# Performance work log

Measured on AMD Instinct MI355X. Metric: run time of the kernel, lower is better.

Reference implementation:

```python
import jax, jax.numpy as jnp
import numpy as np

N_NODES = 50000
N_EDGES = 800000
IN_DIM = 128
HID_DIM = 64
OUT_DIM = 64
NUM_GRAPHS = 512


def setup_inputs() -> dict:
    key = jax.random.key(0)
    ks = jax.random.split(key, 8)
    x = jax.random.normal(ks[0], (N_NODES, IN_DIM), dtype=jnp.float32)
    edge_index = jax.random.randint(ks[1], (2, N_EDGES), 0, N_NODES, dtype=jnp.int64)
    batch = jnp.sort(jax.random.randint(ks[2], (N_NODES,), 0, NUM_GRAPHS, dtype=jnp.int64))
    s1 = 1.0 / np.sqrt(IN_DIM)
    s2 = 1.0 / np.sqrt(HID_DIM)
    W1 = jax.random.uniform(ks[3], (IN_DIM, HID_DIM), jnp.float32, -s1, s1)
    b1 = jax.random.uniform(ks[4], (HID_DIM,), jnp.float32, -s1, s1)
    W2 = jax.random.uniform(ks[5], (HID_DIM, OUT_DIM), jnp.float32, -s2, s2)
    b2 = jax.random.uniform(ks[6], (OUT_DIM,), jnp.float32, -s2, s2)
    return {"x": x, "edge_index": edge_index, "batch": batch,
            "W1": W1, "b1": b1, "W2": W2, "b2": b2}


def _gcn_layer(h, W, b, src, dst, norm, n_nodes):
    # linear transform first (keeps the per-edge gather at output width)
    h = h @ W + b                      # [N, d_out]
    msg = h[src] * norm[:, None]       # [E, d_out] gathered, normalized messages
    agg = jax.ops.segment_sum(msg, dst, num_segments=n_nodes)  # scatter-add
    return jax.nn.relu(agg)


def reference(x, edge_index, batch, W1, b1, W2, b2):
    src, dst = edge_index[0], edge_index[1]
    # symmetric degree normalization: deg^{-1/2}[src] * deg^{-1/2}[dst]
    deg = jax.ops.segment_sum(jnp.ones((src.shape[0],), x.dtype), dst,
                              num_segments=N_NODES)
    dinv = jax.lax.rsqrt(jnp.maximum(deg, 1.0))
    norm = dinv[src] * dinv[dst]       # [E]

    h = _gcn_layer(x, W1, b1, src, dst, norm, N_NODES)   # dropout = identity (eval)
    h = _gcn_layer(h, W2, b2, src, dst, norm, N_NODES)

    # scatter_mean pooling over batch indices
    sums = jax.ops.segment_sum(h, batch, num_segments=NUM_GRAPHS)
    cnts = jax.ops.segment_sum(jnp.ones((N_NODES,), h.dtype), batch,
                               num_segments=NUM_GRAPHS)
    return sums / jnp.maximum(cnts, 1.0)[:, None]        # [NUM_GRAPHS, OUT_DIM]
```

## Files before the change

kernel.cpp:

```cpp
#include <hip/hip_runtime.h>
#include <hip/hip_fp16.h>

#define N_NODES 50000
#define N_EDGES 800000
#define IN_DIM 128
#define NUM_GRAPHS 512
#define CAP 64
#define NB 196
#define BCAP 5120
#define FILL_T 2048
#define NFILL 391
#define GEMM1_BLKS 391
#define GEMM_TILES 1563

typedef unsigned short u16;
typedef unsigned int u32;

__device__ __forceinline__ void acc_row(const uint4& v, float2& aa, float2& ab,
                                        float2& ac, float2& ad) {
    const __half2* hp = reinterpret_cast<const __half2*>(&v);
    float2 f;
    f = __half22float2(hp[0]); aa.x += f.x; aa.y += f.y;
    f = __half22float2(hp[1]); ab.x += f.x; ab.y += f.y;
    f = __half22float2(hp[2]); ac.x += f.x; ac.y += f.y;
    f = __half22float2(hp[3]); ad.x += f.x; ad.y += f.y;
}

__device__ __forceinline__ void gather_node(
    const uint4* __restrict__ H16, const u16* __restrict__ sp, int dg, int lo,
    float2& aa, float2& ab, float2& ac, float2& ad) {
    int i = 0;
    for (; i + 7 < dg; i += 8) {
        ushort4 s4a = *reinterpret_cast<const ushort4*>(sp + i);
        ushort4 s4b = *reinterpret_cast<const ushort4*>(sp + i + 4);
        uint4 v0 = H16[(size_t)s4a.x * 8 + lo];
        uint4 v1 = H16[(size_t)s4a.y * 8 + lo];
        uint4 v2 = H16[(size_t)s4a.z * 8 + lo];
        uint4 v3 = H16[(size_t)s4a.w * 8 + lo];
        uint4 v4 = H16[(size_t)s4b.x * 8 + lo];
        uint4 v5 = H16[(size_t)s4b.y * 8 + lo];
        uint4 v6 = H16[(size_t)s4b.z * 8 + lo];
        uint4 v7 = H16[(size_t)s4b.w * 8 + lo];
        acc_row(v0, aa, ab, ac, ad); acc_row(v1, aa, ab, ac, ad);
        acc_row(v2, aa, ab, ac, ad); acc_row(v3, aa, ab, ac, ad);
        acc_row(v4, aa, ab, ac, ad); acc_row(v5, aa, ab, ac, ad);
        acc_row(v6, aa, ab, ac, ad); acc_row(v7, aa, ab, ac, ad);
    }
    for (; i + 3 < dg; i += 4) {
        ushort4 s4 = *reinterpret_cast<const ushort4*>(sp + i);
        uint4 v0 = H16[(size_t)s4.x * 8 + lo];
        uint4 v1 = H16[(size_t)s4.y * 8 + lo];
        uint4 v2 = H16[(size_t)s4.z * 8 + lo];
        uint4 v3 = H16[(size_t)s4.w * 8 + lo];
        acc_row(v0, aa, ab, ac, ad); acc_row(v1, aa, ab, ac, ad);
        acc_row(v2, aa, ab, ac, ad); acc_row(v3, aa, ab, ac, ad);
    }
    for (; i < dg; ++i) {
        uint4 v = H16[(size_t)sp[i] * 8 + lo];
        acc_row(v, aa, ab, ac, ad);
    }
}

__global__ __launch_bounds__(256) void gemm1_fill_kernel(
    const float* __restrict__ X, const float* __restrict__ W,
    const float* __restrict__ bias, __half* __restrict__ Yh, int n_nodes,
    const int* __restrict__ src, const int* __restrict__ dst,
    int* __restrict__ gcursor, u32* __restrict__ packed, int n_edges) {
    __shared__ float xst[32][128];
    __shared__ float ws[32][64];
    __shared__ int hist[256], cnt2[256], goffs[256];
    const int tid = threadIdx.x;

    if (blockIdx.x & 1) {
        const int fb = blockIdx.x >> 1;
        if (fb >= NFILL) return;
        hist[tid] = 0; cnt2[tid] = 0;
        __syncthreads();
        const int base = fb * FILL_T;
        int d[8], s[8];
#pragma unroll
        for (int i = 0; i < 8; ++i) {
            int e = base + i * 256 + tid;
            if (e < n_edges) {
                d[i] = dst[e]; s[i] = src[e];
                atomicAdd(&hist[d[i] >> 8], 1);
            } else d[i] = -1;
        }
        __syncthreads();
        if (hist[tid] > 0) goffs[tid] = atomicAdd(&gcursor[tid], hist[tid]);
        __syncthreads();
#pragma unroll
        for (int i = 0; i < 8; ++i) {
            if (d[i] >= 0) {
                int b = d[i] >> 8;
                int p = goffs[b] + atomicAdd(&cnt2[b], 1);
                packed[(size_t)b * BCAP + p] = ((u32)d[i] << 16) | (u32)s[i];
            }
        }
        return;
    }

    const int idx = blockIdx.x >> 1;
    const int base = idx * 128;
    const int lane = tid & 63;
    const int w = tid >> 6;
    const int jo = lane & 7;
    const int rg = lane >> 3;
    const int rowb = w * 32 + rg * 4;

    float cc[4][8];
    {
        float4 ba = *reinterpret_cast<const float4*>(bias + jo * 8);
        float4 bb = *reinterpret_cast<const float4*>(bias + jo * 8 + 4);
#pragma unroll
        for (int r = 0; r < 4; ++r) {
            cc[r][0] = ba.x; cc[r][1] = ba.y; cc[r][2] = ba.z; cc[r][3] = ba.w;
            cc[r][4] = bb.x; cc[r][5] = bb.y; cc[r][6] = bb.z; cc[r][7] = bb.w;
        }
    }
    const float4* X4 = reinterpret_cast<const float4*>(X);
    const float4* W4 = reinterpret_cast<const float4*>(W);
    float4* ws4 = reinterpret_cast<float4*>(&ws[0][0]);

    for (int kc = 0; kc < 4; ++kc) {
        if (kc) __syncthreads();
#pragma unroll
        for (int t = 0; t < 4; ++t) {
            int i = t * 256 + tid;
            int row = i >> 3, f4 = i & 7;
            float4 v = make_float4(0.f, 0.f, 0.f, 0.f);
            if (base + row < n_nodes) v = X4[(size_t)(base + row) * 32 + kc * 8 + f4];
            int k0 = f4 * 4;
            xst[k0 + 0][row] = v.x; xst[k0 + 1][row] = v.y;
            xst[k0 + 2][row] = v.z; xst[k0 + 3][row] = v.w;
        }
#pragma unroll
        for (int t = 0; t < 2; ++t)
            ws4[t * 256 + tid] = W4[kc * 512 + t * 256 + tid];
        __syncthreads();

#pragma unroll 8
        for (int kk = 0; kk < 32; ++kk) {
            float4 xv = *reinterpret_cast<const float4*>(&xst[kk][rowb]);
            float4 wa = *reinterpret_cast<const float4*>(&ws[kk][jo * 8]);
            float4 wb = *reinterpret_cast<const float4*>(&ws[kk][jo * 8 + 4]);
            float xr[4] = {xv.x, xv.y, xv.z, xv.w};
            float wv[8] = {wa.x, wa.y, wa.z, wa.w, wb.x, wb.y, wb.z, wb.w};
#pragma unroll
            for (int r = 0; r < 4; ++r)
#pragma unroll
                for (int j = 0; j < 8; ++j) cc[r][j] += xr[r] * wv[j];
        }
    }

#pragma unroll
    for (int r = 0; r < 4; ++r) {
        int row = base + rowb + r;
        if (row < n_nodes) {
            __half2 h0 = __floats2half2_rn(cc[r][0], cc[r][1]);
            __half2 h1 = __floats2half2_rn(cc[r][2], cc[r][3]);
            __half2 h2 = __floats2half2_rn(cc[r][4], cc[r][5]);
            __half2 h3 = __floats2half2_rn(cc[r][6], cc[r][7]);
            uint4 o;
            o.x = *reinterpret_cast<u32*>(&h0); o.y = *reinterpret_cast<u32*>(&h1);
            o.z = *reinterpret_cast<u32*>(&h2); o.w = *reinterpret_cast<u32*>(&h3);
            *reinterpret_cast<uint4*>(Yh + (size_t)row * 64 + jo * 8) = o;
        }
    }
}

__global__ __launch_bounds__(256) void fine_kernel(
    const u32* __restrict__ packed, const int* __restrict__ gcursor,
    u16* __restrict__ ssorted, int* __restrict__ deg, float* __restrict__ dinv,
    __half* __restrict__ H1h,
    const int* __restrict__ batch, int* __restrict__ gstart, int n_graphs) {
    __shared__ u16 image[128 * CAP];
    __shared__ int cur[128];
    __shared__ float ds[128];
    const int tid = threadIdx.x;

    if (blockIdx.x == 2 * NB) {
        for (int g = tid; g <= n_graphs; g += 256) {
            int lo = 0, hi = N_NODES;
            while (lo < hi) {
                int mid = (lo + hi) >> 1;
                if (batch[mid] < g) lo = mid + 1; else hi = mid;
            }
            gstart[g] = lo;
        }
        return;
    }

    const int b = blockIdx.x >> 1;
    const int half = blockIdx.x & 1;
    if (tid < 128) cur[tid] = 0;
    __syncthreads();
    const int cnt = gcursor[b];
    const u32* pp = packed + (size_t)b * BCAP;
    for (int i = tid; i < cnt; i += 256) {
        u32 p = pp[i];
        int dl = (p >> 16) & 255;
        if ((dl >> 7) == half) {
            int loc = dl & 127;
            int pos = atomicAdd(&cur[loc], 1);
            if (pos < CAP) image[loc * CAP + pos] = (u16)(p & 0xffff);
        }
    }
    __syncthreads();
    const int nbase = b * 256 + half * 128;
    if (tid < 128) {
        int c = cur[tid];
        float dv = rsqrtf(fmaxf((float)c, 1.0f));
        ds[tid] = dv;
        int d = nbase + tid;
        if (d < N_NODES) { deg[d] = c; dinv[d] = dv; }
    }
    __syncthreads();
    const u32* im32 = reinterpret_cast<const u32*>(image);
    u32* out32 = reinterpret_cast<u32*>(ssorted) + (size_t)nbase * (CAP / 2);
    for (int i = tid; i < 128 * CAP / 2; i += 256) out32[i] = im32[i];
    __half2* Hp = reinterpret_cast<__half2*>(H1h) + (size_t)nbase * 32;
    const int lim = min(128, N_NODES - nbase) * 32;
    for (int i = tid; i < lim; i += 256) {
        float dv = ds[i >> 5];
        float2 f = __half22float2(Hp[i]);
        Hp[i] = __floats2half2_rn(f.x * dv, f.y * dv);
    }
}

__global__ __launch_bounds__(256) void agg_gemm_kernel(
    const __half* __restrict__ H, const u16* __restrict__ ssorted,
    const int* __restrict__ deg, const float* __restrict__ dinv,
    const float* __restrict__ W, const float* __restrict__ bias,
    __half* __restrict__ Yh, int n_nodes) {
    __shared__ float xs[32][64];
    const int tid = threadIdx.x;
    const int lane = tid & 63;
    const int w = tid >> 6;
    const int lo = lane & 7;
    const int slot = w * 8 + (lane >> 3);
    const int base = blockIdx.x * 32;
    const uint4* H16 = reinterpret_cast<const uint4*>(H);

    int node = base + slot;
    float2 aa = make_float2(0.f, 0.f), ab = make_float2(0.f, 0.f);
    float2 ac = make_float2(0.f, 0.f), ad = make_float2(0.f, 0.f);
    if (node < n_nodes) {
        int dg = min(deg[node], CAP);
        gather_node(H16, ssorted + (size_t)node * CAP, dg, lo, aa, ab, ac, ad);
        float dv = dinv[node];
        *reinterpret_cast<float4*>(&xs[slot][8 * lo]) =
            make_float4(fmaxf(aa.x * dv, 0.f), fmaxf(aa.y * dv, 0.f),
                        fmaxf(ab.x * dv, 0.f), fmaxf(ab.y * dv, 0.f));
        *reinterpret_cast<float4*>(&xs[slot][8 * lo + 4]) =
            make_float4(fmaxf(ac.x * dv, 0.f), fmaxf(ac.y * dv, 0.f),
                        fmaxf(ad.x * dv, 0.f), fmaxf(ad.y * dv, 0.f));
    } else {
        *reinterpret_cast<float4*>(&xs[slot][8 * lo]) = make_float4(0.f, 0.f, 0.f, 0.f);
        *reinterpret_cast<float4*>(&xs[slot][8 * lo + 4]) = make_float4(0.f, 0.f, 0.f, 0.f);
    }
    __syncthreads();

    float b = bias[lane];
    float c[8];
#pragma unroll
    for (int r = 0; r < 8; ++r) c[r] = b;
#pragma unroll 4
    for (int k = 0; k < 64; ++k) {
        float wv = W[k * 64 + lane];
#pragma unroll
        for (int r = 0; r < 8; ++r) c[r] += wv * xs[w * 8 + r][k];
    }
    int n0 = base + w * 8;
#pragma unroll
    for (int r = 0; r < 8; ++r)
        if (n0 + r < n_nodes)
            Yh[(size_t)(n0 + r) * 64 + lane] = __float2half(c[r] * dinv[n0 + r]);
}

__global__ __launch_bounds__(512) void agg2_pool_kernel(
    const __half* __restrict__ H, const u16* __restrict__ ssorted,
    const int* __restrict__ deg, const float* __restrict__ dinv,
    const int* __restrict__ gstart, float* __restrict__ out) {
    __shared__ float part[64][64];
    const int g = blockIdx.x;
    const int tid = threadIdx.x;
    const int lane = tid & 63;
    const int w = tid >> 6;
    const int lo = lane & 7;
    const int slot = w * 8 + (lane >> 3);
    const uint4* H16 = reinterpret_cast<const uint4*>(H);
    const int beg = gstart[g], end = gstart[g + 1];

    float2 pa = make_float2(0.f, 0.f), pb = make_float2(0.f, 0.f);
    float2 pc = make_float2(0.f, 0.f), pd = make_float2(0.f, 0.f);
    for (int node = beg + slot; node < end; node += 64) {
        int dg = min(deg[node], CAP);
        float2 aa = make_float2(0.f, 0.f), ab = make_float2(0.f, 0.f);
        float2 ac = make_float2(0.f, 0.f), ad = make_float2(0.f, 0.f);
        gather_node(H16, ssorted + (size_t)node * CAP, dg, lo, aa, ab, ac, ad);
        float dv = dinv[node];
        pa.x += fmaxf(aa.x * dv, 0.f); pa.y += fmaxf(aa.y * dv, 0.f);
        pb.x += fmaxf(ab.x * dv, 0.f); pb.y += fmaxf(ab.y * dv, 0.f);
        pc.x += fmaxf(ac.x * dv, 0.f); pc.y += fmaxf(ac.y * dv, 0.f);
        pd.x += fmaxf(ad.x * dv, 0.f); pd.y += fmaxf(ad.y * dv, 0.f);
    }
    *reinterpret_cast<float4*>(&part[slot][8 * lo]) = make_float4(pa.x, pa.y, pb.x, pb.y);
    *reinterpret_cast<float4*>(&part[slot][8 * lo + 4]) = make_float4(pc.x, pc.y, pd.x, pd.y);
    __syncthreads();
    if (tid < 64) {
        float s = 0.f;
#pragma unroll
        for (int r = 0; r < 64; ++r) s += part[r][tid];
        out[(size_t)g * 64 + tid] = s / fmaxf((float)(end - beg), 1.0f);
    }
}

extern "C" void kernel_launch(void* const* d_in, const int* in_sizes, int n_in,
                              void* d_out, int out_size, void* d_ws, size_t ws_size,
                              hipStream_t stream) {
    const float* x     = (const float*)d_in[0];
    const int*   ei    = (const int*)d_in[1];
    const int*   batch = (const int*)d_in[2];
    const float* W1    = (const float*)d_in[3];
    const float* b1    = (const float*)d_in[4];
    const float* W2    = (const float*)d_in[5];
    const float* b2    = (const float*)d_in[6];
    float* out = (float*)d_out;

    const int* srcp = ei;
    const int* dstp = ei + N_EDGES;

    __half* H1h     = (__half*)d_ws;
    __half* H2h     = H1h + (size_t)N_NODES * 64;
    float*  dinv    = (float*)(H2h + (size_t)N_NODES * 64);
    int*    deg     = (int*)(dinv + N_NODES);
    u16*    ssorted = (u16*)(deg + N_NODES);
    u32*    packed  = (u32*)(ssorted + (size_t)NB * 256 * CAP);
    int*    gcursor = (int*)(packed + (size_t)NB * BCAP);
    int*    gstart  = gcursor + 256;

    hipMemsetAsync(gcursor, 0, 256 * sizeof(int), stream);

    gemm1_fill_kernel<<<2 * NFILL, 256, 0, stream>>>(
        x, W1, b1, H1h, N_NODES, srcp, dstp, gcursor, packed, N_EDGES);

    fine_kernel<<<2 * NB + 1, 256, 0, stream>>>(
        packed, gcursor, ssorted, deg, dinv, H1h, batch, gstart, NUM_GRAPHS);

    agg_gemm_kernel<<<GEMM_TILES, 256, 0, stream>>>(
        H1h, ssorted, deg, dinv, W2, b2, H2h, N_NODES);

    agg2_pool_kernel<<<NUM_GRAPHS, 512, 0, stream>>>(
        H2h, ssorted, deg, dinv, gstart, out);
}
```

Baseline: 171.4 us.

## Replace two-pass bucketed edge sort with direct per-node atomic scatter

The two-stage build of the per-node source lists goes away: first a bucketed packed array, then a shared-memory image copied out per 256-node bucket. Each edge now does a global atomicAdd on deg[dst] and writes its source id straight into ssorted at that slot. The fine kernel becomes a light scale kernel that computes dinv and scales H1 with 16-byte vector accesses. This removes a full pass over the packed edges plus the image copy, but it adds 800k global atomics with contention and scattered 2-byte writes, and it needs a memset of the whole degree array.

```diff
diff --git a/kernel.cpp b/kernel.cpp
--- a/kernel.cpp
+++ b/kernel.cpp
@@ -6,11 +6,11 @@
 #define IN_DIM 128
 #define NUM_GRAPHS 512
 #define CAP 64
-#define NB 196
-#define BCAP 5120
-#define FILL_T 2048
-#define NFILL 391
+#define NSCAT 782
+#define SCAT_T 1024
 #define GEMM1_BLKS 391
+#define SCALE_ROWS 64
+#define SCALE_BLKS 782
 #define GEMM_TILES 1563
 
 typedef unsigned short u16;
@@ -61,46 +61,32 @@
     }
 }
 
-__global__ __launch_bounds__(256) void gemm1_fill_kernel(
+__global__ __launch_bounds__(256) void gemm1_scatter_kernel(
     const float* __restrict__ X, const float* __restrict__ W,
     const float* __restrict__ bias, __half* __restrict__ Yh, int n_nodes,
     const int* __restrict__ src, const int* __restrict__ dst,
-    int* __restrict__ gcursor, u32* __restrict__ packed, int n_edges) {
+    int* __restrict__ deg, u16* __restrict__ ssorted, int n_edges) {
     __shared__ float xst[32][128];
     __shared__ float ws[32][64];
-    __shared__ int hist[256], cnt2[256], goffs[256];
     const int tid = threadIdx.x;
 
     if (blockIdx.x & 1) {
-        const int fb = blockIdx.x >> 1;
-        if (fb >= NFILL) return;
-        hist[tid] = 0; cnt2[tid] = 0;
-        __syncthreads();
-        const int base = fb * FILL_T;
-        int d[8], s[8];
-#pragma unroll
-        for (int i = 0; i < 8; ++i) {
+        const int sb = blockIdx.x >> 1;
+        const int base = sb * SCAT_T;
+#pragma unroll
+        for (int i = 0; i < 4; ++i) {
             int e = base + i * 256 + tid;
             if (e < n_edges) {
-                d[i] = dst[e]; s[i] = src[e];
-                atomicAdd(&hist[d[i] >> 8], 1);
-            } else d[i] = -1;
-        }
-        __syncthreads();
-        if (hist[tid] > 0) goffs[tid] = atomicAdd(&gcursor[tid], hist[tid]);
-        __syncthreads();
-#pragma unroll
-        for (int i = 0; i < 8; ++i) {
-            if (d[i] >= 0) {
-                int b = d[i] >> 8;
-                int p = goffs[b] + atomicAdd(&cnt2[b], 1);
-                packed[(size_t)b * BCAP + p] = ((u32)d[i] << 16) | (u32)s[i];
+                int d = dst[e], s = src[e];
+                int pos = atomicAdd(&deg[d], 1);
+                if (pos < CAP) ssorted[(size_t)d * CAP + pos] = (u16)s;
             }
         }
         return;
     }
 
     const int idx = blockIdx.x >> 1;
+    if (idx >= GEMM1_BLKS) return;
     const int base = idx * 128;
     const int lane = tid & 63;
     const int w = tid >> 6;
@@ -169,17 +155,14 @@
     }
 }
 
-__global__ __launch_bounds__(256) void fine_kernel(
-    const u32* __restrict__ packed, const int* __restrict__ gcursor,
-    u16* __restrict__ ssorted, int* __restrict__ deg, float* __restrict__ dinv,
+__global__ __launch_bounds__(256) void scale_kernel(
+    const int* __restrict__ deg, float* __restrict__ dinv,
     __half* __restrict__ H1h,
     const int* __restrict__ batch, int* __restrict__ gstart, int n_graphs) {
-    __shared__ u16 image[128 * CAP];
-    __shared__ int cur[128];
-    __shared__ float ds[128];
+    __shared__ float ds[SCALE_ROWS];
     const int tid = threadIdx.x;
 
-    if (blockIdx.x == 2 * NB) {
+    if (blockIdx.x == SCALE_BLKS) {
         for (int g = tid; g <= n_graphs; g += 256) {
             int lo = 0, hi = N_NODES;
             while (lo < hi) {
@@ -191,40 +174,29 @@
         return;
     }
 
-    const int b = blockIdx.x >> 1;
-    const int half = blockIdx.x & 1;
-    if (tid < 128) cur[tid] = 0;
+    const int nbase = blockIdx.x * SCALE_ROWS;
+    if (tid < SCALE_ROWS) {
+        int d = nbase + tid;
+        float dv = 1.0f;
+        if (d < N_NODES) {
+            dv = rsqrtf(fmaxf((float)deg[d], 1.0f));
+            dinv[d] = dv;
+        }
+        ds[tid] = dv;
+    }
     __syncthreads();
-    const int cnt = gcursor[b];
-    const u32* pp = packed + (size_t)b * BCAP;
-    for (int i = tid; i < cnt; i += 256) {
-        u32 p = pp[i];
-        int dl = (p >> 16) & 255;
-        if ((dl >> 7) == half) {
-            int loc = dl & 127;
-            int pos = atomicAdd(&cur[loc], 1);
-            if (pos < CAP) image[loc * CAP + pos] = (u16)(p & 0xffff);
-        }
-    }
-    __syncthreads();
-    const int nbase = b * 256 + half * 128;
-    if (tid < 128) {
-        int c = cur[tid];
-        float dv = rsqrtf(fmaxf((float)c, 1.0f));
-        ds[tid] = dv;
-        int d = nbase + tid;
-        if (d < N_NODES) { deg[d] = c; dinv[d] = dv; }
-    }
-    __syncthreads();
-    const u32* im32 = reinterpret_cast<const u32*>(image);
-    u32* out32 = reinterpret_cast<u32*>(ssorted) + (size_t)nbase * (CAP / 2);
-    for (int i = tid; i < 128 * CAP / 2; i += 256) out32[i] = im32[i];
-    __half2* Hp = reinterpret_cast<__half2*>(H1h) + (size_t)nbase * 32;
-    const int lim = min(128, N_NODES - nbase) * 32;
+    uint4* Hp4 = reinterpret_cast<uint4*>(H1h) + (size_t)nbase * 8;
+    const int lim = min(SCALE_ROWS, N_NODES - nbase) * 8;
     for (int i = tid; i < lim; i += 256) {
-        float dv = ds[i >> 5];
-        float2 f = __half22float2(Hp[i]);
-        Hp[i] = __floats2half2_rn(f.x * dv, f.y * dv);
+        float dv = ds[i >> 3];
+        uint4 v = Hp4[i];
+        __half2* h = reinterpret_cast<__half2*>(&v);
+#pragma unroll
+        for (int j = 0; j < 4; ++j) {
+            float2 f = __half22float2(h[j]);
+            h[j] = __floats2half2_rn(f.x * dv, f.y * dv);
+        }
+        Hp4[i] = v;
     }
 }
 
@@ -336,17 +308,15 @@
     float*  dinv    = (float*)(H2h + (size_t)N_NODES * 64);
     int*    deg     = (int*)(dinv + N_NODES);
     u16*    ssorted = (u16*)(deg + N_NODES);
-    u32*    packed  = (u32*)(ssorted + (size_t)NB * 256 * CAP);
-    int*    gcursor = (int*)(packed + (size_t)NB * BCAP);
-    int*    gstart  = gcursor + 256;
-
-    hipMemsetAsync(gcursor, 0, 256 * sizeof(int), stream);
-
-    gemm1_fill_kernel<<<2 * NFILL, 256, 0, stream>>>(
-        x, W1, b1, H1h, N_NODES, srcp, dstp, gcursor, packed, N_EDGES);
-
-    fine_kernel<<<2 * NB + 1, 256, 0, stream>>>(
-        packed, gcursor, ssorted, deg, dinv, H1h, batch, gstart, NUM_GRAPHS);
+    int*    gstart  = (int*)(ssorted + (size_t)50176 * CAP);
+
+    hipMemsetAsync(deg, 0, N_NODES * sizeof(int), stream);
+
+    gemm1_scatter_kernel<<<2 * NSCAT, 256, 0, stream>>>(
+        x, W1, b1, H1h, N_NODES, srcp, dstp, deg, ssorted, N_EDGES);
+
+    scale_kernel<<<SCALE_BLKS + 1, 256, 0, stream>>>(
+        deg, dinv, H1h, batch, gstart, NUM_GRAPHS);
 
     agg_gemm_kernel<<<GEMM_TILES, 256, 0, stream>>>(
         H1h, ssorted, deg, dinv, W2, b2, H2h, N_NODES);
```

Measured after the change: 177.1 us. 1.03x slower.

## Use 128-node edge buckets, single-pass fill offsets, and split pooling across two blocks

Applied to the files above, without the earlier changes.

Changes edge bucketing from 256-node to 128-node buckets. Each fine block now processes exactly one bucket instead of two half-blocks both scanning the same packed list and discarding half of it. The fill phase records each edge's local slot during the histogram pass, so the second shared-memory atomic pass is gone. Pooling now uses two blocks per graph that combine through atomicAdd into a zeroed output, which raises parallelism at the cost of an extra memset and float atomics. With BCAP reduced, bucket overflow becomes a risk if edges per bucket exceed 2816.

```diff
diff --git a/kernel.cpp b/kernel.cpp
--- a/kernel.cpp
+++ b/kernel.cpp
@@ -6,8 +6,8 @@
 #define IN_DIM 128
 #define NUM_GRAPHS 512
 #define CAP 64
-#define NB 196
-#define BCAP 5120
+#define NB 392
+#define BCAP 2816
 #define FILL_T 2048
 #define NFILL 391
 #define GEMM1_BLKS 391
@@ -68,39 +68,40 @@
     int* __restrict__ gcursor, u32* __restrict__ packed, int n_edges) {
     __shared__ float xst[32][128];
     __shared__ float ws[32][64];
-    __shared__ int hist[256], cnt2[256], goffs[256];
+    __shared__ int cnt2[NB], goffs[NB];
     const int tid = threadIdx.x;
 
     if (blockIdx.x & 1) {
         const int fb = blockIdx.x >> 1;
-        if (fb >= NFILL) return;
-        hist[tid] = 0; cnt2[tid] = 0;
+        for (int i = tid; i < NB; i += 256) cnt2[i] = 0;
         __syncthreads();
         const int base = fb * FILL_T;
-        int d[8], s[8];
+        int d[8], s[8], pl[8];
 #pragma unroll
         for (int i = 0; i < 8; ++i) {
             int e = base + i * 256 + tid;
             if (e < n_edges) {
                 d[i] = dst[e]; s[i] = src[e];
-                atomicAdd(&hist[d[i] >> 8], 1);
+                pl[i] = atomicAdd(&cnt2[d[i] >> 7], 1);
             } else d[i] = -1;
         }
         __syncthreads();
-        if (hist[tid] > 0) goffs[tid] = atomicAdd(&gcursor[tid], hist[tid]);
+        for (int b = tid; b < NB; b += 256)
+            if (cnt2[b] > 0) goffs[b] = atomicAdd(&gcursor[b], cnt2[b]);
         __syncthreads();
 #pragma unroll
         for (int i = 0; i < 8; ++i) {
             if (d[i] >= 0) {
-                int b = d[i] >> 8;
-                int p = goffs[b] + atomicAdd(&cnt2[b], 1);
-                packed[(size_t)b * BCAP + p] = ((u32)d[i] << 16) | (u32)s[i];
+                int b = d[i] >> 7;
+                packed[(size_t)b * BCAP + goffs[b] + pl[i]] =
+                    ((u32)d[i] << 16) | (u32)s[i];
             }
         }
         return;
     }
 
     const int idx = blockIdx.x >> 1;
+    if (idx >= GEMM1_BLKS) return;
     const int base = idx * 128;
     const int lane = tid & 63;
     const int w = tid >> 6;
@@ -179,7 +180,7 @@
     __shared__ float ds[128];
     const int tid = threadIdx.x;
 
-    if (blockIdx.x == 2 * NB) {
+    if (blockIdx.x == NB) {
         for (int g = tid; g <= n_graphs; g += 256) {
             int lo = 0, hi = N_NODES;
             while (lo < hi) {
@@ -191,23 +192,19 @@
         return;
     }
 
-    const int b = blockIdx.x >> 1;
-    const int half = blockIdx.x & 1;
+    const int b = blockIdx.x;
     if (tid < 128) cur[tid] = 0;
     __syncthreads();
     const int cnt = gcursor[b];
     const u32* pp = packed + (size_t)b * BCAP;
     for (int i = tid; i < cnt; i += 256) {
         u32 p = pp[i];
-        int dl = (p >> 16) & 255;
-        if ((dl >> 7) == half) {
-            int loc = dl & 127;
-            int pos = atomicAdd(&cur[loc], 1);
-            if (pos < CAP) image[loc * CAP + pos] = (u16)(p & 0xffff);
-        }
-    }
-    __syncthreads();
-    const int nbase = b * 256 + half * 128;
+        int loc = (p >> 16) & 127;
+        int pos = atomicAdd(&cur[loc], 1);
+        if (pos < CAP) image[loc * CAP + pos] = (u16)(p & 0xffff);
+    }
+    __syncthreads();
+    const int nbase = b * 128;
     if (tid < 128) {
         int c = cur[tid];
         float dv = rsqrtf(fmaxf((float)c, 1.0f));
@@ -283,7 +280,8 @@
     const int* __restrict__ deg, const float* __restrict__ dinv,
     const int* __restrict__ gstart, float* __restrict__ out) {
     __shared__ float part[64][64];
-    const int g = blockIdx.x;
+    const int g = blockIdx.x >> 1;
+    const int half = blockIdx.x & 1;
     const int tid = threadIdx.x;
     const int lane = tid & 63;
     const int w = tid >> 6;
@@ -294,7 +292,7 @@
 
     float2 pa = make_float2(0.f, 0.f), pb = make_float2(0.f, 0.f);
     float2 pc = make_float2(0.f, 0.f), pd = make_float2(0.f, 0.f);
-    for (int node = beg + slot; node < end; node += 64) {
+    for (int node = beg + half * 64 + slot; node < end; node += 128) {
         int dg = min(deg[node], CAP);
         float2 aa = make_float2(0.f, 0.f), ab = make_float2(0.f, 0.f);
         float2 ac = make_float2(0.f, 0.f), ad = make_float2(0.f, 0.f);
@@ -312,7 +310,7 @@
         float s = 0.f;
 #pragma unroll
         for (int r = 0; r < 64; ++r) s += part[r][tid];
-        out[(size_t)g * 64 + tid] = s / fmaxf((float)(end - beg), 1.0f);
+        atomicAdd(&out[(size_t)g * 64 + tid], s / fmaxf((float)(end - beg), 1.0f));
     }
 }
 
@@ -336,21 +334,22 @@
     float*  dinv    = (float*)(H2h + (size_t)N_NODES * 64);
     int*    deg     = (int*)(dinv + N_NODES);
     u16*    ssorted = (u16*)(deg + N_NODES);
-    u32*    packed  = (u32*)(ssorted + (size_t)NB * 256 * CAP);
+    u32*    packed  = (u32*)(ssorted + (size_t)NB * 128 * CAP);
     int*    gcursor = (int*)(packed + (size_t)NB * BCAP);
-    int*    gstart  = gcursor + 256;
-
-    hipMemsetAsync(gcursor, 0, 256 * sizeof(int), stream);
+    int*    gstart  = gcursor + NB;
+
+    hipMemsetAsync(gcursor, 0, NB * sizeof(int), stream);
+    hipMemsetAsync(d_out, 0, out_size, stream);
 
     gemm1_fill_kernel<<<2 * NFILL, 256, 0, stream>>>(
         x, W1, b1, H1h, N_NODES, srcp, dstp, gcursor, packed, N_EDGES);
 
-    fine_kernel<<<2 * NB + 1, 256, 0, stream>>>(
+    fine_kernel<<<NB + 1, 256, 0, stream>>>(
         packed, gcursor, ssorted, deg, dinv, H1h, batch, gstart, NUM_GRAPHS);
 
     agg_gemm_kernel<<<GEMM_TILES, 256, 0, stream>>>(
         H1h, ssorted, deg, dinv, W2, b2, H2h, N_NODES);
 
-    agg2_pool_kernel<<<NUM_GRAPHS, 512, 0, stream>>>(
+    agg2_pool_kernel<<<2 * NUM_GRAPHS, 512, 0, stream>>>(
         H2h, ssorted, deg, dinv, gstart, out);
 }
```

New measurement: 172.1 us. No clear change (+0.4%).
